# Kernel optimization log

Hardware: AMD Instinct MI355X
Metric: run time of the kernel (lower is better)

The kernel has to match this reference:

```python
import jax, jax.numpy as jnp
import numpy as np

B, N, IN_DIM, HEADS, PER_HEAD = 8, 512, 256, 4, 32
OUT_DIM = HEADS * PER_HEAD  # 128
NEG_SLOPE = 0.2


def setup_inputs() -> dict:
    key = jax.random.key(0)
    ks = jax.random.split(key, 8)
    x = jax.random.normal(ks[0], (B, N, IN_DIM), jnp.float32)
    adj = jax.random.randint(ks[1], (B, N, N), 0, 2, jnp.int32)
    sl = 1.0 / np.sqrt(IN_DIM)
    W_l = jax.random.normal(ks[2], (IN_DIM, OUT_DIM), jnp.float32) * sl  # source proj
    b_l = jnp.zeros((OUT_DIM,), jnp.float32)
    W_r = jax.random.normal(ks[3], (IN_DIM, OUT_DIM), jnp.float32) * sl  # target proj
    b_r = jnp.zeros((OUT_DIM,), jnp.float32)
    att = jax.random.normal(ks[4], (HEADS, PER_HEAD), jnp.float32) * (1.0 / np.sqrt(PER_HEAD))
    bias = jnp.zeros((OUT_DIM,), jnp.float32)
    return {"x": x, "adj": adj, "W_l": W_l, "b_l": b_l, "W_r": W_r, "b_r": b_r,
            "att": att, "bias": bias}


def _gatv2_single(x_b, adj_b, W_l, b_l, W_r, b_r, att, bias):
    # PyG GATv2Conv: remove_self_loops + add_self_loops -> diagonal forced to 1
    n = x_b.shape[0]
    adj_sl = jnp.fill_diagonal(adj_b, 1, inplace=False)
    # edge_index = adj.nonzero().t(): source = row, target = col
    m = (adj_sl != 0).T  # m[i, j]: source j feeds target i
    xl = (x_b @ W_l + b_l).reshape(n, HEADS, PER_HEAD)  # source-side features
    xr = (x_b @ W_r + b_r).reshape(n, HEADS, PER_HEAD)  # target-side features
    s = xr[:, None] + xl[None, :]                       # [i, j, H, C]
    s = jnp.where(s > 0, s, NEG_SLOPE * s)              # LeakyReLU(0.2)
    e = jnp.einsum('ijhc,hc->ijh', s, att)              # attention logits
    e = jnp.where(m[..., None], e, -jnp.inf)
    alpha = jax.nn.softmax(e, axis=1)                   # softmax over sources j
    out = jnp.einsum('ijh,jhc->ihc', alpha, xl).reshape(n, HEADS * PER_HEAD)
    return out + bias


def reference(x, adj, W_l, b_l, W_r, b_r, att, bias):
    # Sequential per-batch processing, faithful to the original Python loop
    # and keeping the [N,N,H,C] intermediate to one graph at a time.
    def one(args):
        x_b, adj_b = args
        return _gatv2_single(x_b, adj_b, W_l, b_l, W_r, b_r, att, bias)
    return jax.lax.map(one, (x, adj))  # [B, N, OUT_DIM]
```

## Files before the change

kernel.cpp:

```cpp
#include <hip/hip_runtime.h>
#include <hip/hip_bf16.h>

#define B_   8
#define N_   512
#define IND  256
#define H_   4
#define PH   32
#define OD   128
#define TI   4
#define TJ   64
#define XLS_STRIDE 132

__global__ __launch_bounds__(256, 2) void proj_kernel(
    const float* __restrict__ x,
    const float* __restrict__ Wl, const float* __restrict__ bl,
    const float* __restrict__ Wr, const float* __restrict__ br,
    float* __restrict__ xl, float* __restrict__ xr)
{
    __shared__ float xs[8 * IND];
    const int t = threadIdx.x;
    const int row0 = blockIdx.x * 8;

    const float4* xp4 = (const float4*)(x + (size_t)row0 * IND);
    float4* xs4 = (float4*)xs;
    #pragma unroll
    for (int k = 0; k < 2; ++k)
        xs4[t + k * 256] = xp4[t + k * 256];
    __syncthreads();

    const int which = t >> 7;
    const int rg = (t >> 6) & 1;
    const int og = t & 63;
    const int o0 = og * 2;
    const int r0 = rg * 4;
    const float* W  = which ? Wr : Wl;
    const float* bb = which ? br : bl;

    float acc0[4], acc1[4];
    #pragma unroll
    for (int r = 0; r < 4; ++r) { acc0[r] = 0.f; acc1[r] = 0.f; }

    for (int k = 0; k < IND; k += 4) {
        float wf0[4], wf1[4];
        #pragma unroll
        for (int kk = 0; kk < 4; ++kk) {
            float2 wv = *(const float2*)(W + (size_t)(k + kk) * OD + o0);
            wf0[kk] = wv.x;
            wf1[kk] = wv.y;
        }
        float xv[4][4];
        #pragma unroll
        for (int r = 0; r < 4; ++r)
            *(float4*)(xv[r]) = *(const float4*)(&xs[(r0 + r) * IND + k]);
        #pragma unroll
        for (int kk = 0; kk < 4; ++kk)
            #pragma unroll
            for (int r = 0; r < 4; ++r) {
                acc0[r] = fmaf(xv[r][kk], wf0[kk], acc0[r]);
                acc1[r] = fmaf(xv[r][kk], wf1[kk], acc1[r]);
            }
    }

    const float bv0 = bb[o0];
    const float bv1 = bb[o0 + 1];
    float* dst = which ? xr : xl;
    #pragma unroll
    for (int r = 0; r < 4; ++r) {
        float2 v = make_float2(acc0[r] + bv0, acc1[r] + bv1);
        *(float2*)(&dst[(size_t)(row0 + r0 + r) * OD + o0]) = v;
    }
}

__global__ __launch_bounds__(256, 2) void attn_kernel(
    const int* __restrict__ adj, const float* __restrict__ att,
    const float* __restrict__ bias,
    const float* __restrict__ xl, const float* __restrict__ xr,
    float* __restrict__ out)
{
    __shared__ float xls[TJ * XLS_STRIDE];
    __shared__ float masks[TJ * TI];
    __shared__ float dls[TJ * H_];

    const int t = threadIdx.x;
    const int b  = blockIdx.x >> 7;
    const int i0 = (blockIdx.x & 127) * TI;
    const int ch = t & 1;
    const int q  = (t >> 1) & 7;
    const int h  = (t >> 4) & 3;
    const int il = t >> 6;
    const int ig = i0 + il;
    const int cbase = h * PH + ch * 16;

    float attv[16], xrv[16];
    {
        const float* xrp = xr + ((size_t)(b * N_ + ig)) * OD + cbase;
        #pragma unroll
        for (int k = 0; k < 16; k += 4) {
            float4 v = *(const float4*)(xrp + k);
            xrv[k] = v.x; xrv[k+1] = v.y; xrv[k+2] = v.z; xrv[k+3] = v.w;
        }
        const float* ap = att + cbase;
        #pragma unroll
        for (int k = 0; k < 16; ++k) attv[k] = ap[k];
    }
    float drh = 0.f;
    #pragma unroll
    for (int k = 0; k < 16; ++k) drh = fmaf(attv[k], xrv[k], drh);
    const float dr = drh + __shfl_xor(drh, 1);
    const float c0 = 0.6f * dr;

    float acc[16];
    #pragma unroll
    for (int k = 0; k < 16; ++k) acc[k] = 0.f;
    float sumw = 0.f;

    const float* xlb = xl + (size_t)b * N_ * OD;
    const int* adjb  = adj + (size_t)b * N_ * N_;

    for (int tile = 0; tile < N_ / TJ; ++tile) {
        const int j0 = tile * TJ;
        __syncthreads();
        #pragma unroll
        for (int k = 0; k < 8; ++k) {
            int idx = t + k * 256;
            int jj = idx >> 5, m = idx & 31;
            *(float4*)(&xls[jj * XLS_STRIDE + m * 4]) =
                *(const float4*)(xlb + (size_t)(j0 + jj) * OD + m * 4);
        }
        {
            int jj = t >> 2, ii = t & 3;
            int jg2 = j0 + jj, ig2 = i0 + ii;
            int a = adjb[(size_t)jg2 * N_ + ig2];
            masks[t] = (a != 0 || jg2 == ig2) ? 1.f : 0.f;
        }
        __syncthreads();
        {
            const int jj0 = il * 16 + q * 2;
            const float* p0 = &xls[jj0 * XLS_STRIDE + cbase];
            float s0a = 0.f, s0b = 0.f, s1a = 0.f, s1b = 0.f;
            #pragma unroll
            for (int k = 0; k < 16; k += 2) {
                s0a = fmaf(attv[k],   p0[k],   s0a);
                s0b = fmaf(attv[k+1], p0[k+1], s0b);
                s1a = fmaf(attv[k],   p0[XLS_STRIDE + k],   s1a);
                s1b = fmaf(attv[k+1], p0[XLS_STRIDE + k+1], s1b);
            }
            float s0 = s0a + s0b, s1 = s1a + s1b;
            float o0 = s0 + __shfl_xor(s0, 1);
            float o1 = s1 + __shfl_xor(s1, 1);
            dls[(jj0 + ch) * H_ + h] = ch ? o1 : o0;
        }
        __syncthreads();
        #pragma unroll 2
        for (int u = 0; u < 8; ++u) {
            const int jj = q + u * 8;
            const float* vrow = &xls[jj * XLS_STRIDE + cbase];
            float v[16];
            #pragma unroll
            for (int k = 0; k < 16; k += 4) {
                float4 w4 = *(const float4*)(vrow + k);
                v[k] = w4.x; v[k+1] = w4.y; v[k+2] = w4.z; v[k+3] = w4.w;
            }
            float ea = 0.f, eb = 0.f, ec = 0.f, ed = 0.f;
            #pragma unroll
            for (int k = 0; k < 16; k += 4) {
                ea = fmaf(attv[k+0], fabsf(xrv[k+0] + v[k+0]), ea);
                eb = fmaf(attv[k+1], fabsf(xrv[k+1] + v[k+1]), eb);
                ec = fmaf(attv[k+2], fabsf(xrv[k+2] + v[k+2]), ec);
                ed = fmaf(attv[k+3], fabsf(xrv[k+3] + v[k+3]), ed);
            }
            float e2h = (ea + eb) + (ec + ed);
            float e2 = e2h + __shfl_xor(e2h, 1);
            float e = fmaf(0.6f, dls[jj * H_ + h], c0);
            e = fmaf(0.4f, e2, e);
            float w = masks[jj * TI + il] * __expf(e);
            sumw += w;
            #pragma unroll
            for (int k = 0; k < 16; ++k) acc[k] = fmaf(w, v[k], acc[k]);
        }
    }

    sumw += __shfl_xor(sumw, 2);
    sumw += __shfl_xor(sumw, 4);
    sumw += __shfl_xor(sumw, 8);
    const float inv = 1.f / sumw;

    float r8[8];
    {
        const bool hi = (q & 4) != 0;
        #pragma unroll
        for (int m = 0; m < 8; ++m) {
            float send = hi ? acc[m] : acc[8 + m];
            float keep = hi ? acc[8 + m] : acc[m];
            r8[m] = keep + __shfl_xor(send, 8);
        }
    }
    float r4[4];
    {
        const bool hi = (q & 2) != 0;
        #pragma unroll
        for (int m = 0; m < 4; ++m) {
            float send = hi ? r4[0] : r4[0];
            (void)send;
            float s2 = hi ? r8[m] : r8[4 + m];
            float kp = hi ? r8[4 + m] : r8[m];
            r4[m] = kp + __shfl_xor(s2, 4);
        }
    }
    float r2[2];
    {
        const bool hi = (q & 1) != 0;
        #pragma unroll
        for (int m = 0; m < 2; ++m) {
            float s2 = hi ? r4[m] : r4[2 + m];
            float kp = hi ? r4[2 + m] : r4[m];
            r2[m] = kp + __shfl_xor(s2, 2);
        }
    }

    const int c = cbase + q * 2;
    float* op = out + ((size_t)(b * N_ + ig)) * OD;
    op[c]     = fmaf(r2[0], inv, bias[c]);
    op[c + 1] = fmaf(r2[1], inv, bias[c + 1]);
}

extern "C" void kernel_launch(void* const* d_in, const int* in_sizes, int n_in,
                              void* d_out, int out_size, void* d_ws, size_t ws_size,
                              hipStream_t stream) {
    const float* x    = (const float*)d_in[0];
    const int*   adj  = (const int*)d_in[1];
    const float* Wl   = (const float*)d_in[2];
    const float* bl   = (const float*)d_in[3];
    const float* Wr   = (const float*)d_in[4];
    const float* br   = (const float*)d_in[5];
    const float* att  = (const float*)d_in[6];
    const float* bias = (const float*)d_in[7];
    float* out = (float*)d_out;

    float* xl = (float*)d_ws;
    float* xr = xl + (size_t)B_ * N_ * OD;

    proj_kernel<<<512, 256, 0, stream>>>(x, Wl, bl, Wr, br, xl, xr);
    attn_kernel<<<1024, 256, 0, stream>>>(adj, att, bias, xl, xr, out);
}
```

Baseline: 139.2 us.

## Precompute per-node attention dot products in projection kernel, drop per-tile recompute

The projection kernel now also computes att·xl and att·xr per node and head, using a wave shuffle reduction, and writes them to workspace. The attention kernel reads these values instead of recomputing the dl dot products for every tile of every block, which removes one shared-memory pass and one __syncthreads per tile. Thread mapping is swapped so each wave covers a single head, and the output store becomes a float2. The cost is extra small global loads of dl inside the tile loop and extra workspace.

Measured after the change: 132.7 us. -4.7%, faster.

```diff
diff --git a/kernel.cpp b/kernel.cpp
--- a/kernel.cpp
+++ b/kernel.cpp
@@ -15,7 +15,9 @@
     const float* __restrict__ x,
     const float* __restrict__ Wl, const float* __restrict__ bl,
     const float* __restrict__ Wr, const float* __restrict__ br,
-    float* __restrict__ xl, float* __restrict__ xr)
+    const float* __restrict__ att,
+    float* __restrict__ xl, float* __restrict__ xr,
+    float* __restrict__ dl, float* __restrict__ dr)
 {
     __shared__ float xs[8 * IND];
     const int t = threadIdx.x;
@@ -63,11 +65,29 @@
 
     const float bv0 = bb[o0];
     const float bv1 = bb[o0 + 1];
+    const float a0 = att[o0];
+    const float a1 = att[o0 + 1];
     float* dst = which ? xr : xl;
+    float* dp  = which ? dr : dl;
+    float dcon[4];
     #pragma unroll
     for (int r = 0; r < 4; ++r) {
-        float2 v = make_float2(acc0[r] + bv0, acc1[r] + bv1);
-        *(float2*)(&dst[(size_t)(row0 + r0 + r) * OD + o0]) = v;
+        float y0 = acc0[r] + bv0;
+        float y1 = acc1[r] + bv1;
+        *(float2*)(&dst[(size_t)(row0 + r0 + r) * OD + o0]) = make_float2(y0, y1);
+        dcon[r] = fmaf(a0, y0, a1 * y1);
+    }
+    #pragma unroll
+    for (int m = 1; m < 16; m <<= 1) {
+        #pragma unroll
+        for (int r = 0; r < 4; ++r)
+            dcon[r] += __shfl_xor(dcon[r], m);
+    }
+    if ((og & 15) == 0) {
+        const int h = og >> 4;
+        #pragma unroll
+        for (int r = 0; r < 4; ++r)
+            dp[(size_t)(row0 + r0 + r) * H_ + h] = dcon[r];
     }
 }
 
@@ -75,19 +95,19 @@
     const int* __restrict__ adj, const float* __restrict__ att,
     const float* __restrict__ bias,
     const float* __restrict__ xl, const float* __restrict__ xr,
+    const float* __restrict__ dl, const float* __restrict__ dr,
     float* __restrict__ out)
 {
     __shared__ float xls[TJ * XLS_STRIDE];
     __shared__ float masks[TJ * TI];
-    __shared__ float dls[TJ * H_];
 
     const int t = threadIdx.x;
     const int b  = blockIdx.x >> 7;
     const int i0 = (blockIdx.x & 127) * TI;
     const int ch = t & 1;
     const int q  = (t >> 1) & 7;
-    const int h  = (t >> 4) & 3;
-    const int il = t >> 6;
+    const int il = (t >> 4) & 3;
+    const int h  = t >> 6;
     const int ig = i0 + il;
     const int cbase = h * PH + ch * 16;
 
@@ -103,11 +123,7 @@
         #pragma unroll
         for (int k = 0; k < 16; ++k) attv[k] = ap[k];
     }
-    float drh = 0.f;
-    #pragma unroll
-    for (int k = 0; k < 16; ++k) drh = fmaf(attv[k], xrv[k], drh);
-    const float dr = drh + __shfl_xor(drh, 1);
-    const float c0 = 0.6f * dr;
+    const float c0 = 0.6f * dr[((size_t)(b * N_ + ig)) * H_ + h];
 
     float acc[16];
     #pragma unroll
@@ -115,6 +131,7 @@
     float sumw = 0.f;
 
     const float* xlb = xl + (size_t)b * N_ * OD;
+    const float* dlb = dl + (size_t)b * N_ * H_;
     const int* adjb  = adj + (size_t)b * N_ * N_;
 
     for (int tile = 0; tile < N_ / TJ; ++tile) {
@@ -134,23 +151,10 @@
             masks[t] = (a != 0 || jg2 == ig2) ? 1.f : 0.f;
         }
         __syncthreads();
-        {
-            const int jj0 = il * 16 + q * 2;
-            const float* p0 = &xls[jj0 * XLS_STRIDE + cbase];
-            float s0a = 0.f, s0b = 0.f, s1a = 0.f, s1b = 0.f;
-            #pragma unroll
-            for (int k = 0; k < 16; k += 2) {
-                s0a = fmaf(attv[k],   p0[k],   s0a);
-                s0b = fmaf(attv[k+1], p0[k+1], s0b);
-                s1a = fmaf(attv[k],   p0[XLS_STRIDE + k],   s1a);
-                s1b = fmaf(attv[k+1], p0[XLS_STRIDE + k+1], s1b);
-            }
-            float s0 = s0a + s0b, s1 = s1a + s1b;
-            float o0 = s0 + __shfl_xor(s0, 1);
-            float o1 = s1 + __shfl_xor(s1, 1);
-            dls[(jj0 + ch) * H_ + h] = ch ? o1 : o0;
-        }
-        __syncthreads();
+        float dlv[8];
+        #pragma unroll
+        for (int u = 0; u < 8; ++u)
+            dlv[u] = dlb[(size_t)(j0 + q + u * 8) * H_ + h];
         #pragma unroll 2
         for (int u = 0; u < 8; ++u) {
             const int jj = q + u * 8;
@@ -171,7 +175,7 @@
             }
             float e2h = (ea + eb) + (ec + ed);
             float e2 = e2h + __shfl_xor(e2h, 1);
-            float e = fmaf(0.6f, dls[jj * H_ + h], c0);
+            float e = fmaf(0.6f, dlv[u], c0);
             e = fmaf(0.4f, e2, e);
             float w = masks[jj * TI + il] * __expf(e);
             sumw += w;
@@ -200,11 +204,9 @@
         const bool hi = (q & 2) != 0;
         #pragma unroll
         for (int m = 0; m < 4; ++m) {
-            float send = hi ? r4[0] : r4[0];
-            (void)send;
-            float s2 = hi ? r8[m] : r8[4 + m];
-            float kp = hi ? r8[4 + m] : r8[m];
-            r4[m] = kp + __shfl_xor(s2, 4);
+            float send = hi ? r8[m] : r8[4 + m];
+            float keep = hi ? r8[4 + m] : r8[m];
+            r4[m] = keep + __shfl_xor(send, 4);
         }
     }
     float r2[2];
@@ -212,16 +214,16 @@
         const bool hi = (q & 1) != 0;
         #pragma unroll
         for (int m = 0; m < 2; ++m) {
-            float s2 = hi ? r4[m] : r4[2 + m];
-            float kp = hi ? r4[2 + m] : r4[m];
-            r2[m] = kp + __shfl_xor(s2, 2);
+            float send = hi ? r4[m] : r4[2 + m];
+            float keep = hi ? r4[2 + m] : r4[m];
+            r2[m] = keep + __shfl_xor(send, 2);
         }
     }
 
     const int c = cbase + q * 2;
     float* op = out + ((size_t)(b * N_ + ig)) * OD;
-    op[c]     = fmaf(r2[0], inv, bias[c]);
-    op[c + 1] = fmaf(r2[1], inv, bias[c + 1]);
+    *(float2*)(&op[c]) = make_float2(fmaf(r2[0], inv, bias[c]),
+                                     fmaf(r2[1], inv, bias[c + 1]));
 }
 
 extern "C" void kernel_launch(void* const* d_in, const int* in_sizes, int n_in,
@@ -239,7 +241,9 @@
 
     float* xl = (float*)d_ws;
     float* xr = xl + (size_t)B_ * N_ * OD;
-
-    proj_kernel<<<512, 256, 0, stream>>>(x, Wl, bl, Wr, br, xl, xr);
-    attn_kernel<<<1024, 256, 0, stream>>>(adj, att, bias, xl, xr, out);
+    float* dl = xr + (size_t)B_ * N_ * OD;
+    float* dr = dl + (size_t)B_ * N_ * H_;
+
+    proj_kernel<<<512, 256, 0, stream>>>(x, Wl, bl, Wr, br, att, xl, xr, dl, dr);
+    attn_kernel<<<1024, 256, 0, stream>>>(adj, att, bias, xl, xr, dl, dr, out);
 }
```
